# Performance work log

Measured on AMD Instinct MI355X. Metric: run time of the kernel, lower is better.

The kernel has to match this reference:

```python
import jax, jax.numpy as jnp
import numpy as np

B, T = 64, 512
L, D = 2048, 512


def setup_inputs() -> dict:
    key = jax.random.key(0)
    k1, k2, k3 = jax.random.split(key, 3)
    label_sequences = jax.random.randint(k1, (B, T), 0, L)
    source_embeddings = jax.random.normal(k2, (L, D), dtype=jnp.float32)
    target_embeddings = jax.random.normal(k3, (L, D), dtype=jnp.float32)
    return {
        "label_sequences": label_sequences,
        "source_embeddings": source_embeddings,
        "target_embeddings": target_embeddings,
    }


def reference(label_sequences, source_embeddings, target_embeddings):
    # source_index = labels[:, :-1], target_index = labels[:, 1:]
    src_idx = label_sequences[:, :-1]          # [B, T-1]
    tgt_idx = label_sequences[:, 1:]           # [B, T-1]
    # Gather source embeddings per transition pair: [B, T-1, D]
    src = source_embeddings[src_idx]
    # Logits over all target labels: [B, T-1, L]
    logits = jnp.einsum("btd,ld->btl", src, target_embeddings)
    # Row-wise log_softmax over target labels (dim=1 in torch == last axis here)
    logp = jax.nn.log_softmax(logits, axis=-1)
    # Pick the actual next label's log-probability: [B, T-1]
    scores = jnp.take_along_axis(logp, tgt_idx[..., None], axis=-1)[..., 0]
    return scores
```

## Files before the change

### kernel.cpp

```cpp
#include <hip/hip_runtime.h>
#include <hip/hip_bf16.h>

#define L_CLS 2048
#define D_DIM 512
#define T_SZ  512
#define NT    511
#define NOUT  (64 * NT)
#define NCHUNK 32
#define LOG2E 1.4426950408889634f
#define LN2   0.6931471805599453f
#define SHIFT 128.0f

typedef __attribute__((ext_vector_type(8))) short bf16x8;
typedef __attribute__((ext_vector_type(4))) float f32x4;

static __device__ __forceinline__ short f2bf(float x) {
    return (short)__bfloat16_as_ushort(__float2bfloat16(x));
}

__global__ void conv_bf16(const float* __restrict__ srcE, const float* __restrict__ tgtE,
                          __hip_bfloat16* __restrict__ Sb, __hip_bfloat16* __restrict__ Tb) {
    int i = blockIdx.x * blockDim.x + threadIdx.x;
    if (i >= (L_CLS * D_DIM) / 8) return;
    const f32x4* s4 = reinterpret_cast<const f32x4*>(srcE) + i * 2;
    const f32x4* t4 = reinterpret_cast<const f32x4*>(tgtE) + i * 2;
    f32x4 s0 = s4[0], s1 = s4[1];
    f32x4 t0 = t4[0], t1 = t4[1];
    bf16x8 so, to;
#pragma unroll
    for (int j = 0; j < 4; ++j) {
        so[j] = f2bf(s0[j]); so[j + 4] = f2bf(s1[j]);
        to[j] = f2bf(t0[j]); to[j + 4] = f2bf(t1[j]);
    }
    reinterpret_cast<bf16x8*>(Sb)[i] = so;
    reinterpret_cast<bf16x8*>(Tb)[i] = to;
}

__launch_bounds__(512, 4)
__global__ void gemm_lse_bf16(const __hip_bfloat16* __restrict__ Sb,
                              const __hip_bfloat16* __restrict__ Tb,
                              float* __restrict__ psum,
                              float* __restrict__ M) {
    __shared__ __hip_bfloat16 Blds[64 * 128];

    const int tid  = threadIdx.x;
    const int wave = tid >> 6;
    const int lane = tid & 63;
    const int lr   = lane & 15;
    const int hi   = lane >> 4;
    const int C    = blockIdx.x * 64;
    const int R    = blockIdx.y * 128 + wave * 16;

    f32x4 acc[4];
#pragma unroll
    for (int ct = 0; ct < 4; ++ct) acc[ct] = (f32x4){0.f, 0.f, 0.f, 0.f};

    bf16x8 stg[2], an[4];
#pragma unroll
    for (int i = 0; i < 2; ++i) {
        int p = tid + 512 * i;
        stg[i] = *reinterpret_cast<const bf16x8*>(
            &Tb[(C + (p >> 4)) * D_DIM + (p & 15) * 8]);
    }
#pragma unroll
    for (int ks = 0; ks < 4; ++ks)
        an[ks] = *reinterpret_cast<const bf16x8*>(
            &Sb[(R + lr) * D_DIM + ks * 32 + hi * 8]);

#pragma unroll 1
    for (int s = 0; s < 4; ++s) {
#pragma unroll
        for (int i = 0; i < 2; ++i) {
            int p   = tid + 512 * i;
            int row = p >> 4;
            int e   = (p & 15) * 8;
            *reinterpret_cast<bf16x8*>(
                &Blds[row * 128 + (e ^ ((row & 7) << 3))]) = stg[i];
        }
        bf16x8 a[4];
#pragma unroll
        for (int ks = 0; ks < 4; ++ks) a[ks] = an[ks];
        __syncthreads();

        if (s < 3) {
#pragma unroll
            for (int i = 0; i < 2; ++i) {
                int p = tid + 512 * i;
                stg[i] = *reinterpret_cast<const bf16x8*>(
                    &Tb[(C + (p >> 4)) * D_DIM + (s + 1) * 128 + (p & 15) * 8]);
            }
#pragma unroll
            for (int ks = 0; ks < 4; ++ks)
                an[ks] = *reinterpret_cast<const bf16x8*>(
                    &Sb[(R + lr) * D_DIM + (s + 1) * 128 + ks * 32 + hi * 8]);
        }

#pragma unroll
        for (int ks = 0; ks < 4; ++ks) {
#pragma unroll
            for (int ct = 0; ct < 4; ++ct) {
                int row = ct * 16 + lr;
                int e   = (ks * 32 + hi * 8) ^ ((lr & 7) << 3);
                bf16x8 b = *reinterpret_cast<const bf16x8*>(&Blds[row * 128 + e]);
                acc[ct] = __builtin_amdgcn_mfma_f32_16x16x32_bf16(a[ks], b, acc[ct], 0, 0, 0);
            }
        }
        __syncthreads();
    }

#pragma unroll
    for (int i = 0; i < 4; ++i) {
        size_t rg = (size_t)(R + hi * 4 + i) * L_CLS + C + lr;
#pragma unroll
        for (int ct = 0; ct < 4; ++ct)
            M[rg + ct * 16] = acc[ct][i];
    }
    float p[4];
#pragma unroll
    for (int i = 0; i < 4; ++i) {
        p[i] = 0.f;
#pragma unroll
        for (int ct = 0; ct < 4; ++ct)
            p[i] += exp2f(acc[ct][i] * LOG2E - SHIFT);
    }
#pragma unroll
    for (int off = 1; off < 16; off <<= 1)
#pragma unroll
        for (int i = 0; i < 4; ++i) p[i] += __shfl_xor(p[i], off);
    if (lr == 0) {
#pragma unroll
        for (int i = 0; i < 4; ++i)
            psum[(R + hi * 4 + i) * NCHUNK + blockIdx.x] = p[i];
    }
}

__launch_bounds__(256)
__global__ void scores_gather(const int* __restrict__ labels,
                              const float* __restrict__ psum,
                              const float* __restrict__ M,
                              float* __restrict__ out) {
    int o = blockIdx.x * 256 + threadIdx.x;
    if (o >= NOUT) return;
    int b = o / NT;
    int t = o - b * NT;
    int src = labels[b * T_SZ + t];
    int tgt = labels[b * T_SZ + t + 1];

    const f32x4* pv = reinterpret_cast<const f32x4*>(psum + src * NCHUNK);
    f32x4 sv = pv[0];
#pragma unroll
    for (int c = 1; c < NCHUNK / 4; ++c) {
        f32x4 v = pv[c];
        sv[0] += v[0]; sv[1] += v[1]; sv[2] += v[2]; sv[3] += v[3];
    }
    float S = (sv[0] + sv[1]) + (sv[2] + sv[3]);
    float lse = (log2f(S) + SHIFT) * LN2;
    out[o] = M[(size_t)src * L_CLS + tgt] - lse;
}

extern "C" void kernel_launch(void* const* d_in, const int* in_sizes, int n_in,
                              void* d_out, int out_size, void* d_ws, size_t ws_size,
                              hipStream_t stream) {
    const int*   labels = (const int*)d_in[0];
    const float* srcE   = (const float*)d_in[1];
    const float* tgtE   = (const float*)d_in[2];
    float*       out    = (float*)d_out;

    const size_t tbl = (size_t)L_CLS * D_DIM;
    __hip_bfloat16* Sb = (__hip_bfloat16*)d_ws;
    __hip_bfloat16* Tb = Sb + tbl;
    float* psum = (float*)((char*)d_ws + 2 * tbl * sizeof(__hip_bfloat16));
    float* M    = psum + (size_t)L_CLS * NCHUNK;

    conv_bf16<<<(int)(tbl / 8 + 255) / 256, 256, 0, stream>>>(srcE, tgtE, Sb, Tb);
    gemm_lse_bf16<<<dim3(NCHUNK, 16), 512, 0, stream>>>(Sb, Tb, psum, M);
    scores_gather<<<(NOUT + 255) / 256, 256, 0, stream>>>(labels, psum, M, out);
}
```

Measured before the change: 28.23 us.

## Drop full logits matrix write; recompute target logit via per-pair dot product

```diff
diff --git a/kernel.cpp b/kernel.cpp
--- a/kernel.cpp
+++ b/kernel.cpp
@@ -6,7 +6,7 @@
 #define T_SZ  512
 #define NT    511
 #define NOUT  (64 * NT)
-#define NCHUNK 32
+#define NCHUNK 16
 #define LOG2E 1.4426950408889634f
 #define LN2   0.6931471805599453f
 #define SHIFT 128.0f
@@ -16,6 +16,9 @@
 
 static __device__ __forceinline__ short f2bf(float x) {
     return (short)__bfloat16_as_ushort(__float2bfloat16(x));
+}
+static __device__ __forceinline__ float bits2f(unsigned short u) {
+    union { unsigned int i; float f; } v; v.i = ((unsigned int)u) << 16; return v.f;
 }
 
 __global__ void conv_bf16(const float* __restrict__ srcE, const float* __restrict__ tgtE,
@@ -36,28 +39,27 @@
     reinterpret_cast<bf16x8*>(Tb)[i] = to;
 }
 
-__launch_bounds__(512, 4)
+__launch_bounds__(512)
 __global__ void gemm_lse_bf16(const __hip_bfloat16* __restrict__ Sb,
                               const __hip_bfloat16* __restrict__ Tb,
-                              float* __restrict__ psum,
-                              float* __restrict__ M) {
-    __shared__ __hip_bfloat16 Blds[64 * 128];
+                              float* __restrict__ psum) {
+    __shared__ __hip_bfloat16 Blds[128 * 128];
 
     const int tid  = threadIdx.x;
     const int wave = tid >> 6;
     const int lane = tid & 63;
     const int lr   = lane & 15;
     const int hi   = lane >> 4;
-    const int C    = blockIdx.x * 64;
+    const int C    = blockIdx.x * 128;
     const int R    = blockIdx.y * 128 + wave * 16;
 
-    f32x4 acc[4];
+    f32x4 acc[8];
 #pragma unroll
-    for (int ct = 0; ct < 4; ++ct) acc[ct] = (f32x4){0.f, 0.f, 0.f, 0.f};
+    for (int ct = 0; ct < 8; ++ct) acc[ct] = (f32x4){0.f, 0.f, 0.f, 0.f};
 
-    bf16x8 stg[2], an[4];
+    bf16x8 stg[4], an[4];
 #pragma unroll
-    for (int i = 0; i < 2; ++i) {
+    for (int i = 0; i < 4; ++i) {
         int p = tid + 512 * i;
         stg[i] = *reinterpret_cast<const bf16x8*>(
             &Tb[(C + (p >> 4)) * D_DIM + (p & 15) * 8]);
@@ -70,7 +72,7 @@
 #pragma unroll 1
     for (int s = 0; s < 4; ++s) {
 #pragma unroll
-        for (int i = 0; i < 2; ++i) {
+        for (int i = 0; i < 4; ++i) {
             int p   = tid + 512 * i;
             int row = p >> 4;
             int e   = (p & 15) * 8;
@@ -84,7 +86,7 @@
 
         if (s < 3) {
 #pragma unroll
-            for (int i = 0; i < 2; ++i) {
+            for (int i = 0; i < 4; ++i) {
                 int p = tid + 512 * i;
                 stg[i] = *reinterpret_cast<const bf16x8*>(
                     &Tb[(C + (p >> 4)) * D_DIM + (s + 1) * 128 + (p & 15) * 8]);
@@ -98,7 +100,7 @@
 #pragma unroll
         for (int ks = 0; ks < 4; ++ks) {
 #pragma unroll
-            for (int ct = 0; ct < 4; ++ct) {
+            for (int ct = 0; ct < 8; ++ct) {
                 int row = ct * 16 + lr;
                 int e   = (ks * 32 + hi * 8) ^ ((lr & 7) << 3);
                 bf16x8 b = *reinterpret_cast<const bf16x8*>(&Blds[row * 128 + e]);
@@ -108,19 +110,12 @@
         __syncthreads();
     }
 
-#pragma unroll
-    for (int i = 0; i < 4; ++i) {
-        size_t rg = (size_t)(R + hi * 4 + i) * L_CLS + C + lr;
-#pragma unroll
-        for (int ct = 0; ct < 4; ++ct)
-            M[rg + ct * 16] = acc[ct][i];
-    }
     float p[4];
 #pragma unroll
     for (int i = 0; i < 4; ++i) {
         p[i] = 0.f;
 #pragma unroll
-        for (int ct = 0; ct < 4; ++ct)
+        for (int ct = 0; ct < 8; ++ct)
             p[i] += exp2f(acc[ct][i] * LOG2E - SHIFT);
     }
 #pragma unroll
@@ -135,27 +130,32 @@
 }
 
 __launch_bounds__(256)
-__global__ void scores_gather(const int* __restrict__ labels,
-                              const float* __restrict__ psum,
-                              const float* __restrict__ M,
-                              float* __restrict__ out) {
-    int o = blockIdx.x * 256 + threadIdx.x;
-    if (o >= NOUT) return;
-    int b = o / NT;
-    int t = o - b * NT;
-    int src = labels[b * T_SZ + t];
-    int tgt = labels[b * T_SZ + t + 1];
+__global__ void scores_dot(const int* __restrict__ labels,
+                           const __hip_bfloat16* __restrict__ Sb,
+                           const __hip_bfloat16* __restrict__ Tb,
+                           const float* __restrict__ psum,
+                           float* __restrict__ out) {
+    const int wid  = blockIdx.x * 4 + (threadIdx.x >> 6);
+    const int lane = threadIdx.x & 63;
+    const int b = wid / NT;
+    const int t = wid - b * NT;
+    const int src = labels[b * T_SZ + t];
+    const int tgt = labels[b * T_SZ + t + 1];
 
-    const f32x4* pv = reinterpret_cast<const f32x4*>(psum + src * NCHUNK);
-    f32x4 sv = pv[0];
+    bf16x8 sv = *reinterpret_cast<const bf16x8*>(&Sb[src * D_DIM + lane * 8]);
+    bf16x8 tv = *reinterpret_cast<const bf16x8*>(&Tb[tgt * D_DIM + lane * 8]);
+    float acc = 0.f;
 #pragma unroll
-    for (int c = 1; c < NCHUNK / 4; ++c) {
-        f32x4 v = pv[c];
-        sv[0] += v[0]; sv[1] += v[1]; sv[2] += v[2]; sv[3] += v[3];
+    for (int j = 0; j < 8; ++j)
+        acc += bits2f((unsigned short)sv[j]) * bits2f((unsigned short)tv[j]);
+
+    float ps = (lane < NCHUNK) ? psum[src * NCHUNK + lane] : 0.f;
+#pragma unroll
+    for (int off = 32; off; off >>= 1) {
+        acc += __shfl_xor(acc, off);
+        ps  += __shfl_xor(ps, off);
     }
-    float S = (sv[0] + sv[1]) + (sv[2] + sv[3]);
-    float lse = (log2f(S) + SHIFT) * LN2;
-    out[o] = M[(size_t)src * L_CLS + tgt] - lse;
+    if (lane == 0) out[wid] = acc - (log2f(ps) + SHIFT) * LN2;
 }
 
 extern "C" void kernel_launch(void* const* d_in, const int* in_sizes, int n_in,
@@ -170,9 +170,8 @@
     __hip_bfloat16* Sb = (__hip_bfloat16*)d_ws;
     __hip_bfloat16* Tb = Sb + tbl;
     float* psum = (float*)((char*)d_ws + 2 * tbl * sizeof(__hip_bfloat16));
-    float* M    = psum + (size_t)L_CLS * NCHUNK;
 
     conv_bf16<<<(int)(tbl / 8 + 255) / 256, 256, 0, stream>>>(srcE, tgtE, Sb, Tb);
-    gemm_lse_bf16<<<dim3(NCHUNK, 16), 512, 0, stream>>>(Sb, Tb, psum, M);
-    scores_gather<<<(NOUT + 255) / 256, 256, 0, stream>>>(labels, psum, M, out);
+    gemm_lse_bf16<<<dim3(NCHUNK, 16), 512, 0, stream>>>(Sb, Tb, psum);
+    scores_dot<<<NOUT / 4, 256, 0, stream>>>(labels, Sb, Tb, psum, out);
 }
```

Result: slower. 30.38 us (+7.6%).
